# Performance work log

Hardware: AMD Instinct MI355X
Metric: run time of the kernel (lower is better)

Reference implementation:

```python
import jax, jax.numpy as jnp
import numpy as np

V, D, H, L, B, T = 32000, 1024, 16, 4, 2, 2048
DH = D // H
F = 4 * D
EPS = 1e-5


def setup_inputs() -> dict:
    key = jax.random.key(0)
    ks = jax.random.split(key, 16)
    s = 0.02
    n = lambda k, shape: (jax.random.normal(k, shape, jnp.float32) * s)
    inp = {
        "idx": jax.random.randint(ks[0], (B, T), 0, V, dtype=jnp.int64),
        "tok_emb": n(ks[1], (V, D)),
        "pos_emb": n(ks[2], (1, T, D)),
        # per-layer stacked params; Linear weights stored as (in, out)
        "Wq": n(ks[3], (L, D, D)), "bq": jnp.zeros((L, D)),
        "Wk": n(ks[4], (L, D, D)), "bk": jnp.zeros((L, D)),
        "Wv": n(ks[5], (L, D, D)), "bv": jnp.zeros((L, D)),
        "Wo": n(ks[6], (L, D, D)), "bo": jnp.zeros((L, D)),
        "ln1_g": jnp.ones((L, D)), "ln1_b": jnp.zeros((L, D)),
        "W1": n(ks[7], (L, D, F)), "b1": jnp.zeros((L, F)),
        "W2": n(ks[8], (L, F, D)), "b2": jnp.zeros((L, D)),
        "ln2_g": jnp.ones((L, D)), "ln2_b": jnp.zeros((L, D)),
        "lnf_g": jnp.ones((D,)), "lnf_b": jnp.zeros((D,)),
        "lm_W": n(ks[9], (D, V)),
    }
    return inp


def _ln(x, g, b):
    m = jnp.mean(x, axis=-1, keepdims=True)
    v = jnp.mean(jnp.square(x - m), axis=-1, keepdims=True)
    return (x - m) * jax.lax.rsqrt(v + EPS) * g + b


def _band_attn(x, Wq, bq, Wk, bk, Wv, bv, Wo, bo):
    # width-3 causal band: query t attends to keys {t, t-1, t-2}
    b_, t_, _ = x.shape
    q = (x @ Wq + bq).reshape(b_, t_, H, DH)
    k = (x @ Wk + bk).reshape(b_, t_, H, DH)
    v = (x @ Wv + bv).reshape(b_, t_, H, DH)

    def shift(a, o):  # align key at position t-o with query t
        return jnp.pad(a, ((0, 0), (o, 0), (0, 0), (0, 0)))[:, :t_]

    ks_ = jnp.stack([shift(k, o) for o in range(3)], axis=-2)  # (B,T,H,3,DH)
    vs_ = jnp.stack([shift(v, o) for o in range(3)], axis=-2)
    scale = 1.0 / np.sqrt(DH)
    scores = jnp.einsum('bthd,bthod->btho', q, ks_) * scale       # (B,T,H,3)
    pos = jnp.arange(t_)[None, :, None, None]
    off = jnp.arange(3)[None, None, None, :]
    scores = jnp.where(pos >= off, scores, -jnp.inf)
    p = jax.nn.softmax(scores, axis=-1)
    y = jnp.einsum('btho,bthod->bthd', p, vs_).reshape(b_, t_, D)
    return y @ Wo + bo


def reference(idx, tok_emb, pos_emb, Wq, bq, Wk, bk, Wv, bv, Wo, bo,
              ln1_g, ln1_b, W1, b1, W2, b2, ln2_g, ln2_b, lnf_g, lnf_b, lm_W):
    t_ = idx.shape[1]
    x = tok_emb[idx] + pos_emb[:, :t_, :]
    for i in range(L):
        h = _ln(x, ln1_g[i], ln1_b[i])
        x = x + _band_attn(h, Wq[i], bq[i], Wk[i], bk[i], Wv[i], bv[i], Wo[i], bo[i])
        h = _ln(x, ln2_g[i], ln2_b[i])
        h = jax.nn.gelu(h @ W1[i] + b1[i], approximate=False) @ W2[i] + b2[i]
        x = x + h
    x = _ln(x, lnf_g, lnf_b)
    logits = x @ lm_W
    return logits
```

## Files before the change

kernel.cpp:

```cpp
#include <hip/hip_runtime.h>
#include <cstdint>
#include <cstddef>

#define MROWS   4096
#define TSEQ    2048
#define DMODEL  1024
#define NHEAD   16
#define FFN     4096
#define NVOCAB  32000
#define NLAYER  4

typedef float  f32x4  __attribute__((ext_vector_type(4)));
typedef __bf16 bf16x8 __attribute__((ext_vector_type(8)));

__device__ __forceinline__ unsigned short f2bf(float f) {
    unsigned u = __builtin_bit_cast(unsigned, f);
    u += 0x7fffu + ((u >> 16) & 1u);
    return (unsigned short)(u >> 16);
}

__device__ __forceinline__ float gelu_exact(float v) {
    return 0.5f * v * (1.0f + erff(v * 0.7071067811865476f));
}

__global__ __launch_bounds__(256) void embed_kernel(const int* __restrict__ idx,
                                                    const float* __restrict__ tok,
                                                    const float* __restrict__ pos,
                                                    float* __restrict__ x) {
    int row = blockIdx.x, tid = threadIdx.x;
    int token = idx[row];
    int t = row & (TSEQ - 1);
    float4 a = ((const float4*)(tok + (size_t)token * DMODEL))[tid];
    float4 p = ((const float4*)(pos + (size_t)t * DMODEL))[tid];
    a.x += p.x; a.y += p.y; a.z += p.z; a.w += p.w;
    ((float4*)(x + (size_t)row * DMODEL))[tid] = a;
}

__global__ __launch_bounds__(256) void ln_kernel(const float* __restrict__ x,
                                                 const float* __restrict__ g,
                                                 const float* __restrict__ b,
                                                 unsigned short* __restrict__ out) {
    int row = blockIdx.x, tid = threadIdx.x;
    float4 v = ((const float4*)(x + (size_t)row * DMODEL))[tid];
    float s1 = v.x + v.y + v.z + v.w;
    float s2 = v.x * v.x + v.y * v.y + v.z * v.z + v.w * v.w;
    for (int s = 32; s; s >>= 1) { s1 += __shfl_xor(s1, s); s2 += __shfl_xor(s2, s); }
    __shared__ float red[8];
    int lane = tid & 63, w = tid >> 6;
    if (lane == 0) { red[w] = s1; red[4 + w] = s2; }
    __syncthreads();
    s1 = red[0] + red[1] + red[2] + red[3];
    s2 = red[4] + red[5] + red[6] + red[7];
    float mean = s1 * (1.0f / DMODEL);
    float var  = s2 * (1.0f / DMODEL) - mean * mean;
    float rs   = rsqrtf(var + 1e-5f);
    float4 gv = ((const float4*)g)[tid];
    float4 bv = ((const float4*)b)[tid];
    size_t o = (size_t)row * DMODEL + tid * 4;
    out[o + 0] = f2bf((v.x - mean) * rs * gv.x + bv.x);
    out[o + 1] = f2bf((v.y - mean) * rs * gv.y + bv.y);
    out[o + 2] = f2bf((v.z - mean) * rs * gv.z + bv.z);
    out[o + 3] = f2bf((v.w - mean) * rs * gv.w + bv.w);
}

__global__ __launch_bounds__(256) void transpose_bf16(const float* __restrict__ W,
                                                      unsigned short* __restrict__ WT,
                                                      int K, int ldW) {
    __shared__ float tile[32][33];
    int n0 = blockIdx.x * 32, k0 = blockIdx.y * 32;
    int tx = threadIdx.x, ty = threadIdx.y;
#pragma unroll
    for (int r = 0; r < 4; r++)
        tile[ty + 8 * r][tx] = W[(size_t)(k0 + ty + 8 * r) * ldW + n0 + tx];
    __syncthreads();
#pragma unroll
    for (int r = 0; r < 4; r++)
        WT[(size_t)(n0 + ty + 8 * r) * K + k0 + tx] = f2bf(tile[tx][ty + 8 * r]);
}

__global__ __launch_bounds__(256) void pack_qkv_bias(const float* __restrict__ bq,
                                                     const float* __restrict__ bk,
                                                     const float* __restrict__ bv,
                                                     float* __restrict__ dst) {
    int i = blockIdx.x * 256 + threadIdx.x;
    int l = i / 3072, c = i % 3072;
    float v = (c < 1024) ? bq[l * 1024 + c]
            : (c < 2048) ? bk[l * 1024 + c - 1024]
                         : bv[l * 1024 + c - 2048];
    dst[i] = v;
}

__global__ __launch_bounds__(256) void attn_kernel(const float* __restrict__ qkv,
                                                   unsigned short* __restrict__ y) {
    int wid  = (blockIdx.x * 256 + threadIdx.x) >> 6;
    int lane = threadIdx.x & 63;
    int h = wid & (NHEAD - 1);
    int row = wid >> 4;
    int t = row & (TSEQ - 1);
    const float* base = qkv + (size_t)row * 3072 + h * 64;
    float qd = base[lane];
    float d0 = qd * base[1024 + lane];
    float d1 = (t >= 1) ? qd * base[1024 - 3072 + lane] : 0.0f;
    float d2 = (t >= 2) ? qd * base[1024 - 6144 + lane] : 0.0f;
    for (int s = 32; s; s >>= 1) {
        d0 += __shfl_xor(d0, s); d1 += __shfl_xor(d1, s); d2 += __shfl_xor(d2, s);
    }
    d0 *= 0.125f; d1 *= 0.125f; d2 *= 0.125f;
    float m = d0;
    if (t >= 1) m = fmaxf(m, d1);
    if (t >= 2) m = fmaxf(m, d2);
    float p0 = expf(d0 - m);
    float p1 = (t >= 1) ? expf(d1 - m) : 0.0f;
    float p2 = (t >= 2) ? expf(d2 - m) : 0.0f;
    float den = p0 + p1 + p2;
    float v0 = base[2048 + lane];
    float v1 = (t >= 1) ? base[2048 - 3072 + lane] : 0.0f;
    float v2 = (t >= 2) ? base[2048 - 6144 + lane] : 0.0f;
    float yv = (p0 * v0 + p1 * v1 + p2 * v2) / den;
    y[(size_t)row * DMODEL + h * 64 + lane] = f2bf(yv);
}

__device__ __forceinline__ void stage_tile(const unsigned short* __restrict__ g,
                                           unsigned short* s, int K, int tid) {
#pragma unroll
    for (int i = 0; i < 4; ++i) {
        int t2 = tid + i * 512;
        int row = t2 >> 3;
        int col = ((t2 & 7) ^ (row & 7)) * 8;
        __builtin_amdgcn_global_load_lds(
            (const __attribute__((address_space(1))) void*)(g + (size_t)row * K + col),
            (__attribute__((address_space(3))) void*)(s + (size_t)t2 * 8), 16, 0, 0);
    }
}

template <int EPI>
__global__ __launch_bounds__(512, 2) void gemm256(const unsigned short* __restrict__ A,
                                                  const unsigned short* __restrict__ BT,
                                                  const float* __restrict__ bias,
                                                  const float* __restrict__ res,
                                                  float* __restrict__ outF,
                                                  unsigned short* __restrict__ outB,
                                                  int M, int N, int K, int ldc) {
    __shared__ unsigned short As[2][256 * 64];
    __shared__ unsigned short Bs[2][256 * 64];
    const int tid = threadIdx.x;
    const int lane = tid & 63, wid = tid >> 6;
    const int wr = wid >> 2, wc = wid & 3;
    const int lr = lane & 15, kq = lane >> 4;

    const int nbn = N >> 8;
    const int nwg = gridDim.x;
    int orig = blockIdx.x;
    int q8 = nwg >> 3, r8 = nwg & 7;
    int xcd = orig & 7, lin = orig >> 3;
    int wg = (xcd < r8 ? xcd * (q8 + 1) : r8 * (q8 + 1) + (xcd - r8) * q8) + lin;
    int bm = wg / nbn, bn = wg % nbn;

    const unsigned short* Ab = A + (size_t)bm * 256 * K;
    const unsigned short* Bb = BT + (size_t)bn * 256 * K;

    const int aBase = (wr * 128 + lr) * 64;
    const int bBase = (wc * 64 + lr) * 64;
    const int c0 = ((0 * 4 + kq) ^ (lr & 7)) * 8;
    const int c1 = ((1 * 4 + kq) ^ (lr & 7)) * 8;

    f32x4 acc[8][4] = {};
    const int nt = K >> 6;

    stage_tile(Ab, &As[0][0], K, tid);
    stage_tile(Bb, &Bs[0][0], K, tid);
    asm volatile("s_waitcnt vmcnt(0)" ::: "memory");
    __syncthreads();

    for (int t = 0; t < nt; ++t) {
        const unsigned short* sA = &As[t & 1][0];
        const unsigned short* sB = &Bs[t & 1][0];
        unsigned short* dA = &As[(t + 1) & 1][0];
        unsigned short* dB = &Bs[(t + 1) & 1][0];
        const bool pf = (t + 1) < nt;
        const unsigned short* gA = Ab + (size_t)(t + 1) * 64;
        const unsigned short* gB = Bb + (size_t)(t + 1) * 64;

        bf16x8 bfr[4][2];
#pragma unroll
        for (int n = 0; n < 4; ++n) {
            bfr[n][0] = *reinterpret_cast<const bf16x8*>(sB + bBase + n * 16 * 64 + c0);
            bfr[n][1] = *reinterpret_cast<const bf16x8*>(sB + bBase + n * 16 * 64 + c1);
        }

#pragma unroll
        for (int q = 0; q < 4; ++q) {
            bf16x8 af[2][2];
#pragma unroll
            for (int jm = 0; jm < 2; ++jm) {
                const int ro = aBase + (q * 32 + jm * 16) * 64;
                af[jm][0] = *reinterpret_cast<const bf16x8*>(sA + ro + c0);
                af[jm][1] = *reinterpret_cast<const bf16x8*>(sA + ro + c1);
            }
            if (q == 0 && pf) stage_tile(gA, dA, K, tid);
            if (q == 1 && pf) stage_tile(gB, dB, K, tid);
            __builtin_amdgcn_s_barrier();
            __builtin_amdgcn_s_setprio(1);
#pragma unroll
            for (int jm = 0; jm < 2; ++jm)
#pragma unroll
                for (int n = 0; n < 4; ++n) {
                    acc[q * 2 + jm][n] = __builtin_amdgcn_mfma_f32_16x16x32_bf16(af[jm][0], bfr[n][0], acc[q * 2 + jm][n], 0, 0, 0);
                    acc[q * 2 + jm][n] = __builtin_amdgcn_mfma_f32_16x16x32_bf16(af[jm][1], bfr[n][1], acc[q * 2 + jm][n], 0, 0, 0);
                }
            __builtin_amdgcn_s_setprio(0);
            if (q < 3) __builtin_amdgcn_s_barrier();
        }
        asm volatile("s_waitcnt vmcnt(0)" ::: "memory");
        __syncthreads();
    }

    const int row0 = bm * 256 + wr * 128;
    const int col0 = bn * 256 + wc * 64;
#pragma unroll
    for (int m = 0; m < 8; ++m) {
#pragma unroll
        for (int n = 0; n < 4; ++n) {
            int col = col0 + n * 16 + lr;
            int rbase = row0 + m * 16 + kq * 4;
            float bb = bias ? bias[col] : 0.0f;
#pragma unroll
            for (int j = 0; j < 4; ++j) {
                size_t off = (size_t)(rbase + j) * ldc + col;
                float v = acc[m][n][j] + bb;
                if (EPI == 1) v += res[off];
                if (EPI == 2) {
                    outB[off] = f2bf(gelu_exact(v));
                } else {
                    outF[off] = v;
                }
            }
        }
    }
}

#define BM 128
#define BN 128
#define BK 64

template <int EPI>
__global__ __launch_bounds__(256) void gemm_bf16(const unsigned short* __restrict__ A,
                                                 const unsigned short* __restrict__ BT,
                                                 const float* __restrict__ bias,
                                                 const float* __restrict__ res,
                                                 float* __restrict__ outF,
                                                 unsigned short* __restrict__ outB,
                                                 int M, int N, int K, int ldc) {
    __shared__ unsigned short As[BM * BK];
    __shared__ unsigned short Bs[BN * BK];
    int tid = threadIdx.x;
    int bn = blockIdx.x, bm = blockIdx.y;
    const unsigned short* Ab = A + (size_t)bm * BM * K;
    const unsigned short* Bb = BT + (size_t)bn * BN * K;
    int lane = tid & 63, wid = tid >> 6;
    int wr = wid >> 1, wc = wid & 1;
    int lr = lane & 15;
    int lk = (lane >> 4) * 8;

    f32x4 acc[4][4] = {};

    for (int k0 = 0; k0 < K; k0 += BK) {
#pragma unroll
        for (int j = 0; j < 4; j++) {
            int t2 = tid + j * 256;
            int rowa = t2 >> 3, cb = (t2 & 7) * 8;
            __builtin_amdgcn_global_load_lds(
                (const __attribute__((address_space(1))) void*)(Ab + (size_t)rowa * K + k0 + cb),
                (__attribute__((address_space(3))) void*)(As + t2 * 8), 16, 0, 0);
        }
#pragma unroll
        for (int j = 0; j < 4; j++) {
            int t2 = tid + j * 256;
            int rowb = t2 >> 3, cb = (t2 & 7) * 8;
            __builtin_amdgcn_global_load_lds(
                (const __attribute__((address_space(1))) void*)(Bb + (size_t)rowb * K + k0 + cb),
                (__attribute__((address_space(3))) void*)(Bs + t2 * 8), 16, 0, 0);
        }
        __syncthreads();
#pragma unroll
        for (int kk = 0; kk < 2; kk++) {
            bf16x8 af[4], bfv[4];
#pragma unroll
            for (int m = 0; m < 4; m++)
                af[m] = *reinterpret_cast<const bf16x8*>(&As[(wr * 64 + m * 16 + lr) * BK + kk * 32 + lk]);
#pragma unroll
            for (int n = 0; n < 4; n++)
                bfv[n] = *reinterpret_cast<const bf16x8*>(&Bs[(wc * 64 + n * 16 + lr) * BK + kk * 32 + lk]);
#pragma unroll
            for (int m = 0; m < 4; m++)
#pragma unroll
                for (int n = 0; n < 4; n++)
                    acc[m][n] = __builtin_amdgcn_mfma_f32_16x16x32_bf16(af[m], bfv[n], acc[m][n], 0, 0, 0);
        }
        __syncthreads();
    }

    int col0 = bn * BN + wc * 64;
    int row0 = bm * BM + wr * 64;
#pragma unroll
    for (int m = 0; m < 4; m++) {
#pragma unroll
        for (int n = 0; n < 4; n++) {
            int col = col0 + n * 16 + lr;
            int rbase = row0 + m * 16 + (lane >> 4) * 4;
            float bb = bias ? bias[col] : 0.0f;
#pragma unroll
            for (int j = 0; j < 4; j++) {
                int row = rbase + j;
                size_t off = (size_t)row * ldc + col;
                float v = acc[m][n][j] + bb;
                if (EPI == 1) v += res[off];
                if (EPI == 2) {
                    outB[off] = f2bf(gelu_exact(v));
                } else {
                    outF[off] = v;
                }
            }
        }
    }
}

extern "C" void kernel_launch(void* const* d_in, const int* in_sizes, int n_in,
                              void* d_out, int out_size, void* d_ws, size_t ws_size,
                              hipStream_t stream) {
    const int*   idx  = (const int*)d_in[0];
    const float* tok  = (const float*)d_in[1];
    const float* pos  = (const float*)d_in[2];
    const float* Wq   = (const float*)d_in[3];
    const float* bq   = (const float*)d_in[4];
    const float* Wk   = (const float*)d_in[5];
    const float* bk   = (const float*)d_in[6];
    const float* Wv   = (const float*)d_in[7];
    const float* bv   = (const float*)d_in[8];
    const float* Wo   = (const float*)d_in[9];
    const float* bo   = (const float*)d_in[10];
    const float* ln1g = (const float*)d_in[11];
    const float* ln1b = (const float*)d_in[12];
    const float* W1   = (const float*)d_in[13];
    const float* b1   = (const float*)d_in[14];
    const float* W2   = (const float*)d_in[15];
    const float* b2   = (const float*)d_in[16];
    const float* ln2g = (const float*)d_in[17];
    const float* ln2b = (const float*)d_in[18];
    const float* lnfg = (const float*)d_in[19];
    const float* lnfb = (const float*)d_in[20];
    const float* lmW  = (const float*)d_in[21];

    char* ws = (char*)d_ws;
    unsigned short* wbuf  = (unsigned short*)(ws);
    unsigned short* hbuf  = (unsigned short*)(ws + (16u << 20));
    unsigned short* ybuf  = (unsigned short*)(ws + (24u << 20));
    unsigned short* xfbuf = (unsigned short*)(ws + (32u << 20));
    float*          bqkv  = (float*)(ws + (40u << 20));

    float* outF = (float*)d_out;
    float* xbuf = outF;
    float* qkv  = outF + (size_t)MROWS * DMODEL;
    unsigned short* hidden = (unsigned short*)((char*)d_out + (64ull << 20));

    dim3 tb(32, 8);

    embed_kernel<<<MROWS, 256, 0, stream>>>(idx, tok, pos, xbuf);
    pack_qkv_bias<<<(NLAYER * 3072) / 256, 256, 0, stream>>>(bq, bk, bv, bqkv);

    for (int l = 0; l < NLAYER; l++) {
        const size_t wl = (size_t)l * DMODEL * DMODEL;
        ln_kernel<<<MROWS, 256, 0, stream>>>(xbuf, ln1g + l * DMODEL, ln1b + l * DMODEL, hbuf);

        transpose_bf16<<<dim3(32, 32), tb, 0, stream>>>(Wq + wl, wbuf,                           DMODEL, DMODEL);
        transpose_bf16<<<dim3(32, 32), tb, 0, stream>>>(Wk + wl, wbuf + (size_t)DMODEL * DMODEL, DMODEL, DMODEL);
        transpose_bf16<<<dim3(32, 32), tb, 0, stream>>>(Wv + wl, wbuf + 2ull * DMODEL * DMODEL,  DMODEL, DMODEL);
        gemm256<0><<<dim3((3072 / 256) * (MROWS / 256)), 512, 0, stream>>>(
            hbuf, wbuf, bqkv + l * 3072, nullptr, qkv, nullptr, MROWS, 3072, DMODEL, 3072);

        attn_kernel<<<MROWS * NHEAD / 4, 256, 0, stream>>>(qkv, ybuf);

        transpose_bf16<<<dim3(32, 32), tb, 0, stream>>>(Wo + wl, wbuf, DMODEL, DMODEL);
        gemm_bf16<1><<<dim3(DMODEL / BN, MROWS / BM), 256, 0, stream>>>(
            ybuf, wbuf, bo + l * DMODEL, xbuf, xbuf, nullptr, MROWS, DMODEL, DMODEL, DMODEL);

        ln_kernel<<<MROWS, 256, 0, stream>>>(xbuf, ln2g + l * DMODEL, ln2b + l * DMODEL, hbuf);

        transpose_bf16<<<dim3(FFN / 32, DMODEL / 32), tb, 0, stream>>>(W1 + (size_t)l * DMODEL * FFN, wbuf, DMODEL, FFN);
        gemm256<2><<<dim3((FFN / 256) * (MROWS / 256)), 512, 0, stream>>>(
            hbuf, wbuf, b1 + l * FFN, nullptr, nullptr, hidden, MROWS, FFN, DMODEL, FFN);

        transpose_bf16<<<dim3(DMODEL / 32, FFN / 32), tb, 0, stream>>>(W2 + (size_t)l * FFN * DMODEL, wbuf, FFN, DMODEL);
        gemm_bf16<1><<<dim3(DMODEL / BN, MROWS / BM), 256, 0, stream>>>(
            hidden, wbuf, b2 + l * DMODEL, xbuf, xbuf, nullptr, MROWS, DMODEL, FFN, DMODEL);
    }

    ln_kernel<<<MROWS, 256, 0, stream>>>(xbuf, lnfg, lnfb, xfbuf);

    const int NCHUNK = 6400;
    for (int c = 0; c < NVOCAB / NCHUNK; c++) {
        int n0 = c * NCHUNK;
        transpose_bf16<<<dim3(NCHUNK / 32, DMODEL / 32), tb, 0, stream>>>(lmW + n0, wbuf, DMODEL, NVOCAB);
        gemm256<0><<<dim3((NCHUNK / 256) * (MROWS / 256)), 512, 0, stream>>>(
            xfbuf, wbuf, nullptr, nullptr, outF + n0, nullptr, MROWS, NCHUNK, DMODEL, NVOCAB);
    }
}
```

Measured before the change: 1.584 ms.

## Replace N=1024 GEMMs with pipelined 128-tile kernel, bf16 QKV, wider transpose

Replaces the simple single-buffered 128x128 GEMM used for the output projection and FFN down-projection with a new 512-thread kernel. It uses a triple-buffered LDS pipeline, XOR-swizzled staging, XCD-aware block remapping and setprio around its MFMAs. The QKV GEMM now writes bf16 instead of fp32, so the attention kernel reads half the bytes. The weight transpose kernel moves to 64x64 tiles with float4 loads and ushort4 stores to cut its memory transactions. Storing QKV in bf16 adds rounding to q/k/v before attention.

```diff
diff --git a/kernel.cpp b/kernel.cpp
--- a/kernel.cpp
+++ b/kernel.cpp
@@ -17,6 +17,9 @@
     unsigned u = __builtin_bit_cast(unsigned, f);
     u += 0x7fffu + ((u >> 16) & 1u);
     return (unsigned short)(u >> 16);
+}
+__device__ __forceinline__ float bf2f(unsigned short u) {
+    return __builtin_bit_cast(float, (unsigned)u << 16);
 }
 
 __device__ __forceinline__ float gelu_exact(float v) {
@@ -66,16 +69,33 @@
 __global__ __launch_bounds__(256) void transpose_bf16(const float* __restrict__ W,
                                                       unsigned short* __restrict__ WT,
                                                       int K, int ldW) {
-    __shared__ float tile[32][33];
-    int n0 = blockIdx.x * 32, k0 = blockIdx.y * 32;
-    int tx = threadIdx.x, ty = threadIdx.y;
-#pragma unroll
-    for (int r = 0; r < 4; r++)
-        tile[ty + 8 * r][tx] = W[(size_t)(k0 + ty + 8 * r) * ldW + n0 + tx];
+    __shared__ float tile[64][65];
+    int n0 = blockIdx.x * 64, k0 = blockIdx.y * 64;
+    int tid = threadIdx.x;
+    int lr4 = tid & 15;
+    int rw  = tid >> 4;
+#pragma unroll
+    for (int p = 0; p < 4; ++p) {
+        int k = rw + p * 16;
+        float4 v = *(const float4*)(W + (size_t)(k0 + k) * ldW + n0 + lr4 * 4);
+        tile[k][lr4 * 4 + 0] = v.x;
+        tile[k][lr4 * 4 + 1] = v.y;
+        tile[k][lr4 * 4 + 2] = v.z;
+        tile[k][lr4 * 4 + 3] = v.w;
+    }
     __syncthreads();
-#pragma unroll
-    for (int r = 0; r < 4; r++)
-        WT[(size_t)(n0 + ty + 8 * r) * K + k0 + tx] = f2bf(tile[tx][ty + 8 * r]);
+    int kc = tid & 15;
+    int nr = tid >> 4;
+#pragma unroll
+    for (int p = 0; p < 4; ++p) {
+        int n = nr + p * 16;
+        ushort4 o;
+        o.x = f2bf(tile[kc * 4 + 0][n]);
+        o.y = f2bf(tile[kc * 4 + 1][n]);
+        o.z = f2bf(tile[kc * 4 + 2][n]);
+        o.w = f2bf(tile[kc * 4 + 3][n]);
+        *(ushort4*)(WT + (size_t)(n0 + n) * K + k0 + kc * 4) = o;
+    }
 }
 
 __global__ __launch_bounds__(256) void pack_qkv_bias(const float* __restrict__ bq,
@@ -90,18 +110,18 @@
     dst[i] = v;
 }
 
-__global__ __launch_bounds__(256) void attn_kernel(const float* __restrict__ qkv,
+__global__ __launch_bounds__(256) void attn_kernel(const unsigned short* __restrict__ qkv,
                                                    unsigned short* __restrict__ y) {
     int wid  = (blockIdx.x * 256 + threadIdx.x) >> 6;
     int lane = threadIdx.x & 63;
     int h = wid & (NHEAD - 1);
     int row = wid >> 4;
     int t = row & (TSEQ - 1);
-    const float* base = qkv + (size_t)row * 3072 + h * 64;
-    float qd = base[lane];
-    float d0 = qd * base[1024 + lane];
-    float d1 = (t >= 1) ? qd * base[1024 - 3072 + lane] : 0.0f;
-    float d2 = (t >= 2) ? qd * base[1024 - 6144 + lane] : 0.0f;
+    const unsigned short* base = qkv + (size_t)row * 3072 + h * 64;
+    float qd = bf2f(base[lane]);
+    float d0 = qd * bf2f(base[1024 + lane]);
+    float d1 = (t >= 1) ? qd * bf2f(base[1024 - 3072 + lane]) : 0.0f;
+    float d2 = (t >= 2) ? qd * bf2f(base[1024 - 6144 + lane]) : 0.0f;
     for (int s = 32; s; s >>= 1) {
         d0 += __shfl_xor(d0, s); d1 += __shfl_xor(d1, s); d2 += __shfl_xor(d2, s);
     }
@@ -113,9 +133,9 @@
     float p1 = (t >= 1) ? expf(d1 - m) : 0.0f;
     float p2 = (t >= 2) ? expf(d2 - m) : 0.0f;
     float den = p0 + p1 + p2;
-    float v0 = base[2048 + lane];
-    float v1 = (t >= 1) ? base[2048 - 3072 + lane] : 0.0f;
-    float v2 = (t >= 2) ? base[2048 - 6144 + lane] : 0.0f;
+    float v0 = bf2f(base[2048 + lane]);
+    float v1 = (t >= 1) ? bf2f(base[2048 - 3072 + lane]) : 0.0f;
+    float v2 = (t >= 2) ? bf2f(base[2048 - 6144 + lane]) : 0.0f;
     float yv = (p0 * v0 + p1 * v1 + p2 * v2) / den;
     y[(size_t)row * DMODEL + h * 64 + lane] = f2bf(yv);
 }
@@ -229,97 +249,129 @@
                 size_t off = (size_t)(rbase + j) * ldc + col;
                 float v = acc[m][n][j] + bb;
                 if (EPI == 1) v += res[off];
-                if (EPI == 2) {
-                    outB[off] = f2bf(gelu_exact(v));
-                } else {
-                    outF[off] = v;
+                if (EPI == 2)      outB[off] = f2bf(gelu_exact(v));
+                else if (EPI == 3) outB[off] = f2bf(v);
+                else               outF[off] = v;
+            }
+        }
+    }
+}
+
+__device__ __forceinline__ void stage128(const unsigned short* __restrict__ g,
+                                         unsigned short* s, int K, int tid) {
+#pragma unroll
+    for (int i = 0; i < 2; ++i) {
+        int t2 = tid + i * 512;
+        int row = t2 >> 3;
+        int col = ((t2 & 7) ^ (row & 7)) * 8;
+        __builtin_amdgcn_global_load_lds(
+            (const __attribute__((address_space(1))) void*)(g + (size_t)row * K + col),
+            (__attribute__((address_space(3))) void*)(s + (size_t)t2 * 8), 16, 0, 0);
+    }
+}
+
+template <int EPI>
+__global__ __launch_bounds__(512, 2) void gemm128(const unsigned short* __restrict__ A,
+                                                  const unsigned short* __restrict__ BT,
+                                                  const float* __restrict__ bias,
+                                                  const float* __restrict__ res,
+                                                  float* __restrict__ outF,
+                                                  unsigned short* __restrict__ outB,
+                                                  int M, int N, int K, int ldc) {
+    __shared__ unsigned short As[3][128 * 64];
+    __shared__ unsigned short Bs[3][128 * 64];
+    const int tid = threadIdx.x;
+    const int lane = tid & 63, wid = tid >> 6;
+    const int wr = wid >> 2, wc = wid & 3;
+    const int lr = lane & 15, kq = lane >> 4;
+
+    const int nbn = N >> 7;
+    const int nwg = gridDim.x;
+    int orig = blockIdx.x;
+    int q8 = nwg >> 3, r8 = nwg & 7;
+    int xcd = orig & 7, lin = orig >> 3;
+    int wg = (xcd < r8 ? xcd * (q8 + 1) : r8 * (q8 + 1) + (xcd - r8) * q8) + lin;
+    int bm = wg / nbn, bn = wg % nbn;
+
+    const unsigned short* Ab = A + (size_t)bm * 128 * K;
+    const unsigned short* Bb = BT + (size_t)bn * 128 * K;
+
+    const int aBase = (wr * 64 + lr) * 64;
+    const int bBase = (wc * 32 + lr) * 64;
+    const int c0 = (kq ^ (lr & 7)) * 8;
+    const int c1 = ((4 + kq) ^ (lr & 7)) * 8;
+
+    f32x4 acc[4][2] = {};
+    const int nt = K >> 6;
+
+    stage128(Ab,      &As[0][0], K, tid);
+    stage128(Bb,      &Bs[0][0], K, tid);
+    stage128(Ab + 64, &As[1][0], K, tid);
+    stage128(Bb + 64, &Bs[1][0], K, tid);
+    asm volatile("s_waitcnt vmcnt(4)" ::: "memory");
+    __builtin_amdgcn_s_barrier();
+
+    for (int t = 0; t < nt; ++t) {
+        const unsigned short* sA = &As[t % 3][0];
+        const unsigned short* sB = &Bs[t % 3][0];
+        const bool pf = (t + 2) < nt;
+        unsigned short* dA = &As[(t + 2) % 3][0];
+        unsigned short* dB = &Bs[(t + 2) % 3][0];
+        const unsigned short* gA = Ab + (size_t)(t + 2) * 64;
+        const unsigned short* gB = Bb + (size_t)(t + 2) * 64;
+
+        bf16x8 bfr[2][2];
+#pragma unroll
+        for (int n = 0; n < 2; ++n) {
+            bfr[n][0] = *reinterpret_cast<const bf16x8*>(sB + bBase + n * 16 * 64 + c0);
+            bfr[n][1] = *reinterpret_cast<const bf16x8*>(sB + bBase + n * 16 * 64 + c1);
+        }
+#pragma unroll
+        for (int p = 0; p < 2; ++p) {
+            bf16x8 af[2][2];
+#pragma unroll
+            for (int jm = 0; jm < 2; ++jm) {
+                const int ro = aBase + ((p * 2 + jm) * 16) * 64;
+                af[jm][0] = *reinterpret_cast<const bf16x8*>(sA + ro + c0);
+                af[jm][1] = *reinterpret_cast<const bf16x8*>(sA + ro + c1);
+            }
+            if (pf && p == 0) stage128(gA, dA, K, tid);
+            if (pf && p == 1) stage128(gB, dB, K, tid);
+            __builtin_amdgcn_s_barrier();
+            __builtin_amdgcn_s_setprio(1);
+#pragma unroll
+            for (int jm = 0; jm < 2; ++jm)
+#pragma unroll
+                for (int n = 0; n < 2; ++n) {
+                    acc[p * 2 + jm][n] = __builtin_amdgcn_mfma_f32_16x16x32_bf16(af[jm][0], bfr[n][0], acc[p * 2 + jm][n], 0, 0, 0);
+                    acc[p * 2 + jm][n] = __builtin_amdgcn_mfma_f32_16x16x32_bf16(af[jm][1], bfr[n][1], acc[p * 2 + jm][n], 0, 0, 0);
                 }
-            }
-        }
-    }
-}
-
-#define BM 128
-#define BN 128
-#define BK 64
-
-template <int EPI>
-__global__ __launch_bounds__(256) void gemm_bf16(const unsigned short* __restrict__ A,
-                                                 const unsigned short* __restrict__ BT,
-                                                 const float* __restrict__ bias,
-                                                 const float* __restrict__ res,
-                                                 float* __restrict__ outF,
-                                                 unsigned short* __restrict__ outB,
-                                                 int M, int N, int K, int ldc) {
-    __shared__ unsigned short As[BM * BK];
-    __shared__ unsigned short Bs[BN * BK];
-    int tid = threadIdx.x;
-    int bn = blockIdx.x, bm = blockIdx.y;
-    const unsigned short* Ab = A + (size_t)bm * BM * K;
-    const unsigned short* Bb = BT + (size_t)bn * BN * K;
-    int lane = tid & 63, wid = tid >> 6;
-    int wr = wid >> 1, wc = wid & 1;
-    int lr = lane & 15;
-    int lk = (lane >> 4) * 8;
-
-    f32x4 acc[4][4] = {};
-
-    for (int k0 = 0; k0 < K; k0 += BK) {
-#pragma unroll
-        for (int j = 0; j < 4; j++) {
-            int t2 = tid + j * 256;
-            int rowa = t2 >> 3, cb = (t2 & 7) * 8;
-            __builtin_amdgcn_global_load_lds(
-                (const __attribute__((address_space(1))) void*)(Ab + (size_t)rowa * K + k0 + cb),
-                (__attribute__((address_space(3))) void*)(As + t2 * 8), 16, 0, 0);
-        }
-#pragma unroll
-        for (int j = 0; j < 4; j++) {
-            int t2 = tid + j * 256;
-            int rowb = t2 >> 3, cb = (t2 & 7) * 8;
-            __builtin_amdgcn_global_load_lds(
-                (const __attribute__((address_space(1))) void*)(Bb + (size_t)rowb * K + k0 + cb),
-                (__attribute__((address_space(3))) void*)(Bs + t2 * 8), 16, 0, 0);
-        }
-        __syncthreads();
-#pragma unroll
-        for (int kk = 0; kk < 2; kk++) {
-            bf16x8 af[4], bfv[4];
-#pragma unroll
-            for (int m = 0; m < 4; m++)
-                af[m] = *reinterpret_cast<const bf16x8*>(&As[(wr * 64 + m * 16 + lr) * BK + kk * 32 + lk]);
-#pragma unroll
-            for (int n = 0; n < 4; n++)
-                bfv[n] = *reinterpret_cast<const bf16x8*>(&Bs[(wc * 64 + n * 16 + lr) * BK + kk * 32 + lk]);
-#pragma unroll
-            for (int m = 0; m < 4; m++)
-#pragma unroll
-                for (int n = 0; n < 4; n++)
-                    acc[m][n] = __builtin_amdgcn_mfma_f32_16x16x32_bf16(af[m], bfv[n], acc[m][n], 0, 0, 0);
-        }
-        __syncthreads();
-    }
-
-    int col0 = bn * BN + wc * 64;
-    int row0 = bm * BM + wr * 64;
-#pragma unroll
-    for (int m = 0; m < 4; m++) {
-#pragma unroll
-        for (int n = 0; n < 4; n++) {
+            __builtin_amdgcn_s_setprio(0);
+        }
+        if (t + 1 < nt) {
+            if (pf) asm volatile("s_waitcnt vmcnt(4)" ::: "memory");
+            else    asm volatile("s_waitcnt vmcnt(0)" ::: "memory");
+            __builtin_amdgcn_s_barrier();
+        }
+    }
+
+    const int row0 = bm * 128 + wr * 64;
+    const int col0 = bn * 128 + wc * 32;
+#pragma unroll
+    for (int m = 0; m < 4; ++m) {
+#pragma unroll
+        for (int n = 0; n < 2; ++n) {
             int col = col0 + n * 16 + lr;
-            int rbase = row0 + m * 16 + (lane >> 4) * 4;
+            int rbase = row0 + m * 16 + kq * 4;
             float bb = bias ? bias[col] : 0.0f;
 #pragma unroll
-            for (int j = 0; j < 4; j++) {
-                int row = rbase + j;
-                size_t off = (size_t)row * ldc + col;
+            for (int j = 0; j < 4; ++j) {
+                size_t off = (size_t)(rbase + j) * ldc + col;
                 float v = acc[m][n][j] + bb;
                 if (EPI == 1) v += res[off];
-                if (EPI == 2) {
-                    outB[off] = f2bf(gelu_exact(v));
-                } else {
-                    outF[off] = v;
-                }
+                if (EPI == 2)      outB[off] = f2bf(gelu_exact(v));
+                else if (EPI == 3) outB[off] = f2bf(v);
+                else               outF[off] = v;
             }
         }
     }
@@ -360,10 +412,8 @@
 
     float* outF = (float*)d_out;
     float* xbuf = outF;
-    float* qkv  = outF + (size_t)MROWS * DMODEL;
+    unsigned short* qkv = (unsigned short*)((char*)d_out + (16ull << 20));
     unsigned short* hidden = (unsigned short*)((char*)d_out + (64ull << 20));
-
-    dim3 tb(32, 8);
 
     embed_kernel<<<MROWS, 256, 0, stream>>>(idx, tok, pos, xbuf);
     pack_qkv_bias<<<(NLAYER * 3072) / 256, 256, 0, stream>>>(bq, bk, bv, bqkv);
@@ -372,26 +422,26 @@
         const size_t wl = (size_t)l * DMODEL * DMODEL;
         ln_kernel<<<MROWS, 256, 0, stream>>>(xbuf, ln1g + l * DMODEL, ln1b + l * DMODEL, hbuf);
 
-        transpose_bf16<<<dim3(32, 32), tb, 0, stream>>>(Wq + wl, wbuf,                           DMODEL, DMODEL);
-        transpose_bf16<<<dim3(32, 32), tb, 0, stream>>>(Wk + wl, wbuf + (size_t)DMODEL * DMODEL, DMODEL, DMODEL);
-        transpose_bf16<<<dim3(32, 32), tb, 0, stream>>>(Wv + wl, wbuf + 2ull * DMODEL * DMODEL,  DMODEL, DMODEL);
-        gemm256<0><<<dim3((3072 / 256) * (MROWS / 256)), 512, 0, stream>>>(
-            hbuf, wbuf, bqkv + l * 3072, nullptr, qkv, nullptr, MROWS, 3072, DMODEL, 3072);
+        transpose_bf16<<<dim3(16, 16), 256, 0, stream>>>(Wq + wl, wbuf,                           DMODEL, DMODEL);
+        transpose_bf16<<<dim3(16, 16), 256, 0, stream>>>(Wk + wl, wbuf + (size_t)DMODEL * DMODEL, DMODEL, DMODEL);
+        transpose_bf16<<<dim3(16, 16), 256, 0, stream>>>(Wv + wl, wbuf + 2ull * DMODEL * DMODEL,  DMODEL, DMODEL);
+        gemm256<3><<<dim3((3072 / 256) * (MROWS / 256)), 512, 0, stream>>>(
+            hbuf, wbuf, bqkv + l * 3072, nullptr, nullptr, qkv, MROWS, 3072, DMODEL, 3072);
 
         attn_kernel<<<MROWS * NHEAD / 4, 256, 0, stream>>>(qkv, ybuf);
 
-        transpose_bf16<<<dim3(32, 32), tb, 0, stream>>>(Wo + wl, wbuf, DMODEL, DMODEL);
-        gemm_bf16<1><<<dim3(DMODEL / BN, MROWS / BM), 256, 0, stream>>>(
+        transpose_bf16<<<dim3(16, 16), 256, 0, stream>>>(Wo + wl, wbuf, DMODEL, DMODEL);
+        gemm128<1><<<dim3((DMODEL / 128) * (MROWS / 128)), 512, 0, stream>>>(
             ybuf, wbuf, bo + l * DMODEL, xbuf, xbuf, nullptr, MROWS, DMODEL, DMODEL, DMODEL);
 
         ln_kernel<<<MROWS, 256, 0, stream>>>(xbuf, ln2g + l * DMODEL, ln2b + l * DMODEL, hbuf);
 
-        transpose_bf16<<<dim3(FFN / 32, DMODEL / 32), tb, 0, stream>>>(W1 + (size_t)l * DMODEL * FFN, wbuf, DMODEL, FFN);
+        transpose_bf16<<<dim3(FFN / 64, DMODEL / 64), 256, 0, stream>>>(W1 + (size_t)l * DMODEL * FFN, wbuf, DMODEL, FFN);
         gemm256<2><<<dim3((FFN / 256) * (MROWS / 256)), 512, 0, stream>>>(
             hbuf, wbuf, b1 + l * FFN, nullptr, nullptr, hidden, MROWS, FFN, DMODEL, FFN);
 
-        transpose_bf16<<<dim3(DMODEL / 32, FFN / 32), tb, 0, stream>>>(W2 + (size_t)l * FFN * DMODEL, wbuf, FFN, DMODEL);
-        gemm_bf16<1><<<dim3(DMODEL / BN, MROWS / BM), 256, 0, stream>>>(
+        transpose_bf16<<<dim3(DMODEL / 64, FFN / 64), 256, 0, stream>>>(W2 + (size_t)l * FFN * DMODEL, wbuf, FFN, DMODEL);
+        gemm128<1><<<dim3((DMODEL / 128) * (MROWS / 128)), 512, 0, stream>>>(
             hidden, wbuf, b2 + l * DMODEL, xbuf, xbuf, nullptr, MROWS, DMODEL, FFN, DMODEL);
     }
 
@@ -400,7 +450,7 @@
     const int NCHUNK = 6400;
     for (int c = 0; c < NVOCAB / NCHUNK; c++) {
         int n0 = c * NCHUNK;
-        transpose_bf16<<<dim3(NCHUNK / 32, DMODEL / 32), tb, 0, stream>>>(lmW + n0, wbuf, DMODEL, NVOCAB);
+        transpose_bf16<<<dim3(NCHUNK / 64, DMODEL / 64), 256, 0, stream>>>(lmW + n0, wbuf, DMODEL, NVOCAB);
         gemm256<0><<<dim3((NCHUNK / 256) * (MROWS / 256)), 512, 0, stream>>>(
             xfbuf, wbuf, nullptr, nullptr, outF + n0, nullptr, MROWS, NCHUNK, DMODEL, NVOCAB);
     }
```

Result: faster. 1.447 ms (-8.6%).
